# Kernel optimization log

Measured on AMD Instinct MI355X. Metric: run time of the kernel, lower is better.

The kernel has to match this reference:

```python
import jax, jax.numpy as jnp
import numpy as np

VOCAB = 100000
EMB = 128
B = 16384
P = 4
N = 20
EPS = 1e-3


def setup_inputs() -> dict:
    key = jax.random.key(0)
    k1, k2, k3, k4, k5 = jax.random.split(key, 5)
    return {
        "x": jax.random.randint(k1, (B,), 0, VOCAB),
        "positive_samples": jax.random.randint(k2, (B, P), 0, VOCAB),
        "negative_samples": jax.random.randint(k3, (B, N), 0, VOCAB),
        "emb_table": jax.random.normal(k4, (VOCAB, EMB), dtype=jnp.float32) * 0.02,
        "out_weight": jax.random.normal(k5, (VOCAB, EMB), dtype=jnp.float32) * 0.02,
    }


def reference(x, positive_samples, negative_samples, emb_table, out_weight):
    emb = emb_table[x]  # [B, D]
    ctx_w = out_weight[positive_samples]  # [B, P, D] gather
    neg_w = out_weight[negative_samples]  # [B, N, D] gather
    # batched dot products (torch.bmm with emb.unsqueeze(-1))
    pos_logits = jnp.einsum("bpd,bd->bp", ctx_w, emb)
    neg_logits = jnp.einsum("bnd,bd->bn", neg_w, emb)
    pos_out = jax.nn.sigmoid(pos_logits)
    neg_out = jax.nn.sigmoid(neg_logits)
    positive_loss = -jnp.mean(jnp.log(pos_out))
    negative_loss = -jnp.mean(jnp.log(1.0 - neg_out + EPS))
    return positive_loss + negative_loss
```

## Files before the change

kernel.cpp:

```cpp
#include <hip/hip_runtime.h>
#include <math.h>

#define VOCAB 100000
#define EMB 128
#define BATCH 16384
#define NPOS 4
#define NNEG 20
#define NSAMP (NPOS + NNEG)
#define EPSV 1e-3f

#define NTHREADS 256
#define WPB (NTHREADS / 64)
#define NBLOCKS (BATCH / WPB)

__global__ __launch_bounds__(NTHREADS, 8) void w2v_main(
    const int* __restrict__ x,
    const int* __restrict__ pos,
    const int* __restrict__ neg,
    const float* __restrict__ emb,
    const float* __restrict__ outw,
    float* __restrict__ partials)
{
    const int tid  = threadIdx.x;
    const int lane = tid & 63;
    const int wid  = tid >> 6;
    const int li   = lane & 31;

    const int b = __builtin_amdgcn_readfirstlane((int)(blockIdx.x * WPB + wid));

    const int xb = x[b];
    const int* pb = pos + b * NPOS;
    const int* nb = neg + b * NNEG;

    int sidx[NSAMP];
#pragma unroll
    for (int s = 0; s < NSAMP; ++s)
        sidx[s] = (s < NPOS) ? pb[s] : nb[s - NPOS];

    const float4 e = ((const float4*)(emb + ((long)xb << 7)))[li];

    float pacc = 0.0f, nacc = 0.0f;

#pragma unroll
    for (int k = 0; k < 3; ++k) {
        float4 w[8];
#pragma unroll
        for (int j = 0; j < 8; ++j)
            w[j] = ((const float4*)(outw + ((long)sidx[k * 8 + j] << 7)))[li];

        float d[8];
#pragma unroll
        for (int j = 0; j < 8; ++j)
            d[j] = e.x * w[j].x + e.y * w[j].y + e.z * w[j].z + e.w * w[j].w;

#pragma unroll
        for (int j = 0; j < 8; ++j) {
            d[j] += __shfl_xor(d[j], 1);
            d[j] += __shfl_xor(d[j], 2);
            d[j] += __shfl_xor(d[j], 4);
            d[j] += __shfl_xor(d[j], 8);
            d[j] += __shfl_xor(d[j], 16);
        }

        if (lane < 8) {
            float zz = d[0];
#pragma unroll
            for (int j = 1; j < 8; ++j) zz = (lane == j) ? d[j] : zz;
            const int s = k * 8 + lane;
            const float sg = 1.0f / (1.0f + __expf(-zz));
            if (s < NPOS) pacc += __logf(sg);
            else          nacc += __logf(1.0f - sg + EPSV);
        }
    }

    pacc += __shfl_xor(pacc, 1); pacc += __shfl_xor(pacc, 2); pacc += __shfl_xor(pacc, 4);
    nacc += __shfl_xor(nacc, 1); nacc += __shfl_xor(nacc, 2); nacc += __shfl_xor(nacc, 4);

    __shared__ float sp[WPB];
    __shared__ float sn[WPB];
    if (lane == 0) { sp[wid] = pacc; sn[wid] = nacc; }
    __syncthreads();
    if (tid == 0) {
        float tp = 0.0f, tn = 0.0f;
#pragma unroll
        for (int w2 = 0; w2 < WPB; ++w2) { tp += sp[w2]; tn += sn[w2]; }
        ((float2*)partials)[blockIdx.x] = make_float2(tp, tn);
    }
}

__global__ __launch_bounds__(1024) void w2v_final(
    const float* __restrict__ partials, float* __restrict__ out)
{
    const int tid  = threadIdx.x;
    const int lane = tid & 63;
    const int wid  = tid >> 6;

    float tp = 0.0f, tn = 0.0f;
    for (int k = tid; k < NBLOCKS; k += 1024) {
        const float2 v = ((const float2*)partials)[k];
        tp += v.x;
        tn += v.y;
    }
#pragma unroll
    for (int m = 1; m < 64; m <<= 1) {
        tp += __shfl_xor(tp, m);
        tn += __shfl_xor(tn, m);
    }
    __shared__ float sp[16];
    __shared__ float sn[16];
    if (lane == 0) { sp[wid] = tp; sn[wid] = tn; }
    __syncthreads();
    if (tid == 0) {
        float fp = 0.0f, fn = 0.0f;
#pragma unroll
        for (int w2 = 0; w2 < 16; ++w2) { fp += sp[w2]; fn += sn[w2]; }
        out[0] = -fp / (float)(BATCH * NPOS) - fn / (float)(BATCH * NNEG);
    }
}

extern "C" void kernel_launch(void* const* d_in, const int* in_sizes, int n_in,
                              void* d_out, int out_size, void* d_ws, size_t ws_size,
                              hipStream_t stream) {
    const int*   x    = (const int*)d_in[0];
    const int*   pos  = (const int*)d_in[1];
    const int*   neg  = (const int*)d_in[2];
    const float* emb  = (const float*)d_in[3];
    const float* outw = (const float*)d_in[4];
    float* out = (float*)d_out;
    float* partials = (float*)d_ws;

    w2v_main<<<NBLOCKS, NTHREADS, 0, stream>>>(x, pos, neg, emb, outw, partials);
    w2v_final<<<1, 1024, 0, stream>>>(partials, out);
}
```

Before: 39.98 us.

## Split wavefront into 8-lane groups, each handling one sample row

```diff
diff --git a/kernel.cpp b/kernel.cpp
--- a/kernel.cpp
+++ b/kernel.cpp
@@ -13,7 +13,11 @@
 #define WPB (NTHREADS / 64)
 #define NBLOCKS (BATCH / WPB)
 
-__global__ __launch_bounds__(NTHREADS, 8) void w2v_main(
+__device__ __forceinline__ float dot4(float4 a, float4 b) {
+    return a.x * b.x + a.y * b.y + a.z * b.z + a.w * b.w;
+}
+
+__global__ __launch_bounds__(NTHREADS, 4) void w2v_main(
     const int* __restrict__ x,
     const int* __restrict__ pos,
     const int* __restrict__ neg,
@@ -24,57 +28,53 @@
     const int tid  = threadIdx.x;
     const int lane = tid & 63;
     const int wid  = tid >> 6;
-    const int li   = lane & 31;
+    const int sg   = lane >> 3;
+    const int c    = lane & 7;
 
-    const int b = __builtin_amdgcn_readfirstlane((int)(blockIdx.x * WPB + wid));
+    const int b  = blockIdx.x * WPB + wid;
+    const int xb = x[b];
 
-    const int xb = x[b];
-    const int* pb = pos + b * NPOS;
-    const int* nb = neg + b * NNEG;
+    int idx0, idx1, idx2;
+    {
+        const int j0 = sg;
+        idx0 = (j0 < NPOS) ? pos[b * NPOS + j0] : neg[b * NNEG + (j0 - NPOS)];
+        idx1 = neg[b * NNEG + (8  + sg - NPOS)];
+        idx2 = neg[b * NNEG + (16 + sg - NPOS)];
+    }
 
-    int sidx[NSAMP];
-#pragma unroll
-    for (int s = 0; s < NSAMP; ++s)
-        sidx[s] = (s < NPOS) ? pb[s] : nb[s - NPOS];
-
-    const float4 e = ((const float4*)(emb + ((long)xb << 7)))[li];
+    const float4* er = (const float4*)(emb + ((long)xb << 7));
+    const float4 e0 = er[c];
+    const float4 e1 = er[c + 8];
+    const float4 e2 = er[c + 16];
+    const float4 e3 = er[c + 24];
 
     float pacc = 0.0f, nacc = 0.0f;
 
 #pragma unroll
-    for (int k = 0; k < 3; ++k) {
-        float4 w[8];
-#pragma unroll
-        for (int j = 0; j < 8; ++j)
-            w[j] = ((const float4*)(outw + ((long)sidx[k * 8 + j] << 7)))[li];
+    for (int g = 0; g < 3; ++g) {
+        const int row = (g == 0) ? idx0 : ((g == 1) ? idx1 : idx2);
+        const float4* wr = (const float4*)(outw + ((long)row << 7));
+        const float4 w0 = wr[c];
+        const float4 w1 = wr[c + 8];
+        const float4 w2 = wr[c + 16];
+        const float4 w3 = wr[c + 24];
 
-        float d[8];
-#pragma unroll
-        for (int j = 0; j < 8; ++j)
-            d[j] = e.x * w[j].x + e.y * w[j].y + e.z * w[j].z + e.w * w[j].w;
+        float d = dot4(e0, w0) + dot4(e1, w1) + dot4(e2, w2) + dot4(e3, w3);
 
-#pragma unroll
-        for (int j = 0; j < 8; ++j) {
-            d[j] += __shfl_xor(d[j], 1);
-            d[j] += __shfl_xor(d[j], 2);
-            d[j] += __shfl_xor(d[j], 4);
-            d[j] += __shfl_xor(d[j], 8);
-            d[j] += __shfl_xor(d[j], 16);
-        }
+        d += __shfl_xor(d, 1);
+        d += __shfl_xor(d, 2);
+        d += __shfl_xor(d, 4);
 
-        if (lane < 8) {
-            float zz = d[0];
-#pragma unroll
-            for (int j = 1; j < 8; ++j) zz = (lane == j) ? d[j] : zz;
-            const int s = k * 8 + lane;
-            const float sg = 1.0f / (1.0f + __expf(-zz));
-            if (s < NPOS) pacc += __logf(sg);
-            else          nacc += __logf(1.0f - sg + EPSV);
+        if (c == 0) {
+            const int s = g * 8 + sg;
+            const float sig = 1.0f / (1.0f + __expf(-d));
+            if (s < NPOS) pacc += __logf(sig);
+            else          nacc += __logf(1.0f - sig + EPSV);
         }
     }
 
-    pacc += __shfl_xor(pacc, 1); pacc += __shfl_xor(pacc, 2); pacc += __shfl_xor(pacc, 4);
-    nacc += __shfl_xor(nacc, 1); nacc += __shfl_xor(nacc, 2); nacc += __shfl_xor(nacc, 4);
+    pacc += __shfl_xor(pacc, 8); pacc += __shfl_xor(pacc, 16); pacc += __shfl_xor(pacc, 32);
+    nacc += __shfl_xor(nacc, 8); nacc += __shfl_xor(nacc, 16); nacc += __shfl_xor(nacc, 32);
 
     __shared__ float sp[WPB];
     __shared__ float sn[WPB];
@@ -83,7 +83,7 @@
     if (tid == 0) {
         float tp = 0.0f, tn = 0.0f;
 #pragma unroll
-        for (int w2 = 0; w2 < WPB; ++w2) { tp += sp[w2]; tn += sn[w2]; }
+        for (int w = 0; w < WPB; ++w) { tp += sp[w]; tn += sn[w]; }
         ((float2*)partials)[blockIdx.x] = make_float2(tp, tn);
     }
 }
@@ -113,7 +113,7 @@
     if (tid == 0) {
         float fp = 0.0f, fn = 0.0f;
 #pragma unroll
-        for (int w2 = 0; w2 < 16; ++w2) { fp += sp[w2]; fn += sn[w2]; }
+        for (int w = 0; w < 16; ++w) { fp += sp[w]; fn += sn[w]; }
         out[0] = -fp / (float)(BATCH * NPOS) - fn / (float)(BATCH * NNEG);
     }
 }
```

Result: faster. 36.47 us (-8.8%).
